# Kernel tuning notes

Measured on AMD Instinct MI355X. Metric: run time of the kernel, lower is better.

Reference implementation:

```python
import jax, jax.numpy as jnp
import numpy as np

# Constants matching init_kwargs
PC_MIN_X, PC_MIN_Y = -70.4, -40.0
VX, VY = 0.1, 0.1
RADII = (0.4, 0.8)
NSAMPLE = 16
EPS = 1e-5

B, K, N = 2, 2048, 16384
C_BEV, H_BEV, W_BEV = 256, 100, 176


def setup_inputs() -> dict:
    key = jax.random.key(0)
    ks = jax.random.split(key, 16)
    u = lambda k, s: jax.random.uniform(k, s, jnp.float32)
    kp = jnp.stack([
        u(ks[0], (B, K)) * 136.0 - 68.0,
        u(ks[1], (B, K)) * 76.0 - 38.0,
        u(ks[2], (B, K)) * 2.5 - 2.0,   # z in (-2.0, 0.5) -> kpt_mask all True
    ], axis=-1)
    pts = jnp.stack([
        u(ks[3], (B, N)) * 140.0 - 70.0,
        u(ks[4], (B, N)) * 80.0 - 40.0,
        u(ks[5], (B, N)) * 4.0 - 3.0,
    ], axis=-1)
    r = lambda k, s: jax.random.normal(k, s, jnp.float32)
    s01 = lambda k, s: r(k, s) * 0.1
    return {
        "keypoints": kp,
        "points_xyz": pts,
        "points_feat": r(ks[6], (B, N, 1)),
        "spatial_features": r(ks[7], (B, C_BEV, H_BEV, W_BEV)),
        "bev_stride": 8,
        "W0_s0": s01(ks[8], (16, 4)), "g0_s0": jnp.ones(16), "b0_s0": jnp.zeros(16),
        "W1_s0": s01(ks[9], (16, 16)), "g1_s0": jnp.ones(16), "b1_s0": jnp.zeros(16),
        "W0_s1": s01(ks[10], (16, 4)), "g0_s1": jnp.ones(16), "b0_s1": jnp.zeros(16),
        "W1_s1": s01(ks[11], (32, 16)), "g1_s1": jnp.ones(32), "b1_s1": jnp.zeros(32),
        "Wf": s01(ks[12], (128, 304)), "gf": jnp.ones(128), "bf": jnp.zeros(128),
    }


def _batchnorm(x, g, b, axes):
    m = x.mean(axes, keepdims=True)
    v = x.var(axes, keepdims=True)
    return (x - m) * jax.lax.rsqrt(v + EPS) * g + b


def _ball_group(dist2, xyz_b, feat_b, kp_b, radius, ns):
    """pcdet ball_query: first ns in-radius neighbors (index order), pad by first idx."""
    Kq, Np = dist2.shape
    within = dist2 < radius * radius                      # (K, N)
    order = jnp.cumsum(within, axis=1) - 1                # slot for each point
    valid = within & (order < ns)
    pos = jnp.where(valid, order, ns)                     # invalid -> overflow slot
    idx = jnp.zeros((Kq, ns + 1), jnp.int32)
    idx = idx.at[jnp.arange(Kq)[:, None], pos].set(
        jnp.broadcast_to(jnp.arange(Np, dtype=jnp.int32)[None, :], (Kq, Np)))
    idx = idx[:, :ns]
    cnt = within.sum(axis=1)
    slot_ok = jnp.arange(ns)[None, :] < cnt[:, None]
    idx = jnp.where(slot_ok, idx, idx[:, :1])             # replicate first found idx
    empty = cnt == 0
    grouped_xyz = xyz_b[idx] - kp_b[:, None, :]           # (K, ns, 3)
    grouped = jnp.concatenate([grouped_xyz, feat_b[idx]], axis=-1)  # (K, ns, 3+C)
    grouped = jnp.where(empty[:, None, None], 0.0, grouped)
    return grouped, empty


def _group_both_scales(xyz_b, feat_b, kp_b):
    # pairwise dist computed ONCE, shared across both radii
    dist2 = jnp.sum((kp_b[:, None, :] - xyz_b[None, :, :]) ** 2, axis=-1)  # (K, N)
    g0, e0 = _ball_group(dist2, xyz_b, feat_b, kp_b, RADII[0], NSAMPLE)
    g1, e1 = _ball_group(dist2, xyz_b, feat_b, kp_b, RADII[1], NSAMPLE)
    return g0, e0, g1, e1


def _shared_mlp_pool(grouped, empty, layers):
    x = grouped                                            # (B, K, ns, Cin)
    for (W, g, b) in layers:
        x = jnp.einsum('bknc,oc->bkno', x, W)
        x = _batchnorm(x, g, b, axes=(0, 1, 2))            # BN2d over stacked M*ns
        x = jax.nn.relu(x)
    pooled = x.max(axis=2)                                 # max over ns -> (B, K, Cout)
    return jnp.where(empty[:, :, None], 0.0, pooled)


def _bev_interp(bev, kp, stride):
    # bev: (B, C, H, W); kp: (B, K, 3)
    im = jnp.transpose(bev, (0, 2, 3, 1))                  # (B, H, W, C)
    x = (kp[..., 0] - PC_MIN_X) / VX / stride
    y = (kp[..., 1] - PC_MIN_Y) / VY / stride
    Hh, Ww = im.shape[1], im.shape[2]
    x0 = jnp.clip(jnp.floor(x).astype(jnp.int32), 0, Ww - 1)
    x1 = jnp.clip(jnp.floor(x).astype(jnp.int32) + 1, 0, Ww - 1)
    y0 = jnp.clip(jnp.floor(y).astype(jnp.int32), 0, Hh - 1)
    y1 = jnp.clip(jnp.floor(y).astype(jnp.int32) + 1, 0, Hh - 1)
    bidx = jnp.arange(im.shape[0])[:, None]
    Ia, Ib = im[bidx, y0, x0], im[bidx, y1, x0]
    Ic, Id = im[bidx, y0, x1], im[bidx, y1, x1]
    x0f, x1f = x0.astype(x.dtype), x1.astype(x.dtype)
    y0f, y1f = y0.astype(y.dtype), y1.astype(y.dtype)
    wa = ((x1f - x) * (y1f - y))[..., None]
    wb = ((x1f - x) * (y - y0f))[..., None]
    wc = ((x - x0f) * (y1f - y))[..., None]
    wd = ((x - x0f) * (y - y0f))[..., None]
    return Ia * wa + Ib * wb + Ic * wc + Id * wd           # (B, K, C)


def reference(keypoints, points_xyz, points_feat, spatial_features, bev_stride,
              W0_s0, g0_s0, b0_s0, W1_s0, g1_s0, b1_s0,
              W0_s1, g0_s1, b0_s1, W1_s1, g1_s1, b1_s1,
              Wf, gf, bf):
    Bb, Kk, _ = keypoints.shape
    # BEV bilinear interpolation
    bev_feat = _bev_interp(spatial_features, keypoints, bev_stride)  # (B, K, C_bev)
    # per-batch ball-query grouping (vmapped over batch)
    g0, e0, g1, e1 = jax.vmap(_group_both_scales)(points_xyz, points_feat, keypoints)
    p0 = _shared_mlp_pool(g0, e0, [(W0_s0, g0_s0, b0_s0), (W1_s0, g1_s0, b1_s0)])
    p1 = _shared_mlp_pool(g1, e1, [(W0_s1, g0_s1, b0_s1), (W1_s1, g1_s1, b1_s1)])
    pooled = jnp.concatenate([p0, p1], axis=-1)            # (B, K, 48)
    feats = jnp.concatenate([bev_feat, pooled], axis=-1).reshape(Bb * Kk, -1)  # (M, 304)
    # vsa_point_feature_fusion: Linear(no bias) + BN1d(train) + ReLU
    fused = feats @ Wf.T
    fused = jax.nn.relu(_batchnorm(fused, gf, bf, axes=(0,)))
    return fused                                           # (B*K, 128)
```

## Files before the change

kernel.cpp:

```cpp
#include <hip/hip_runtime.h>
#include <hip/hip_bf16.h>

#define NB    2
#define NK    2048
#define NPTS  16384
#define NBK   4096
#define MSAMP 65536.0f
#define MROW  4096.0f

#define NCELLX 176
#define NCELLY 101
#define NCELLS 17776
#define CAP    24

#define NREP   32
#define NCTR   64

#define AL(p) __hip_atomic_load((p), __ATOMIC_RELAXED, __HIP_MEMORY_SCOPE_AGENT)

#define ATOMIC_ADD_ACK(p, v) do { \
  float _r = atomicAdd((p), (v)); \
  asm volatile("" :: "v"(_r)); } while (0)

#define ACC14(M, w, X, Y, Z, F) do { \
  M[0] += (w)*(X); M[1] += (w)*(Y); M[2] += (w)*(Z); M[3] += (w)*(F); \
  M[4] += (w)*(X)*(X); M[5] += (w)*(X)*(Y); M[6] += (w)*(X)*(Z); M[7] += (w)*(X)*(F); \
  M[8] += (w)*(Y)*(Y); M[9] += (w)*(Y)*(Z); M[10] += (w)*(Y)*(F); \
  M[11] += (w)*(Z)*(Z); M[12] += (w)*(Z)*(F); M[13] += (w)*(F)*(F); } while (0)

__device__ __forceinline__ int cell_of(float x, float y) {
  int cx = (int)floorf((x + 70.4f) * 1.25f);
  int cy = (int)floorf((y + 40.0f) * 1.25f);
  cx = min(max(cx, 0), NCELLX - 1);
  cy = min(max(cy, 0), NCELLY - 1);
  return cy * NCELLX + cx;
}

__device__ __forceinline__ void grid_barrier(int* base, int per, int myc) {
  asm volatile("s_waitcnt vmcnt(0)" ::: "memory");
  __syncthreads();
  const int t = threadIdx.x;
  int* ctr = base;
  int* rel = base + NCTR;
  if (t == 0) {
    int old = __hip_atomic_fetch_add(&ctr[myc], 1, __ATOMIC_RELAXED,
                                     __HIP_MEMORY_SCOPE_AGENT);
    asm volatile("" :: "v"(old));
  }
  if (blockIdx.x == 0) {
    if (t < NCTR) {
      while (AL(&ctr[t]) < per) __builtin_amdgcn_s_sleep(8);
    }
    __syncthreads();
    if (t < NCTR)
      __hip_atomic_store(&rel[t], 1, __ATOMIC_RELAXED,
                         __HIP_MEMORY_SCOPE_AGENT);
  } else {
    if (t == 0) {
      while (AL(&rel[myc]) == 0) __builtin_amdgcn_s_sleep(8);
    }
  }
  __syncthreads();
}

__global__ __launch_bounds__(256) void bintrans_kernel(
    const float* __restrict__ pts, const float* __restrict__ pfeat,
    const float* __restrict__ bev,
    int* __restrict__ cellcnt, float4* __restrict__ bucketP,
    int* __restrict__ bucketI, float* __restrict__ bevT)
{
  __shared__ __align__(16) float ttile[64][65];
  const int t = threadIdx.x;
  const int wave = t >> 6;
  const int lane = t & 63;

  if (blockIdx.x < 128) {
    const int i  = blockIdx.x * 256 + t;
    const int b  = i >> 14;
    const int il = i & (NPTS - 1);
    const float* px = pts + (size_t)b * NPTS * 3;
    const float x = px[il*3+0], y = px[il*3+1], z = px[il*3+2];
    const float f = pfeat[(size_t)b * NPTS + il];
    const int c = b * NCELLS + cell_of(x, y);
    const int pos = atomicAdd(&cellcnt[c], 1);
    if (pos < CAP) {
      bucketP[(size_t)c * CAP + pos] = make_float4(x, y, z, f);
      bucketI[(size_t)c * CAP + pos] = il;
    }
    return;
  }

  const int tb  = blockIdx.x - 128;
  const int b   = tb / 1100;
  const int rem = tb % 1100;
  const int cg  = (rem / 275) * 64;
  const int sp0 = (rem % 275) * 64;
  #pragma unroll 4
  for (int i = 0; i < 16; i++) {
    const int c = cg + wave * 16 + i;
    ttile[wave * 16 + i][lane] = bev[((size_t)(b * 256 + c)) * 17600 + sp0 + lane];
  }
  __syncthreads();
  #pragma unroll 4
  for (int i = 0; i < 16; i++) {
    const int s = wave * 16 + i;
    bevT[((size_t)b * 17600 + sp0 + s) * 256 + cg + lane] = ttile[lane][s];
  }
}

__global__ __launch_bounds__(256, 2) void fused_kernel(
    const float* __restrict__ kp, const int* __restrict__ stridep,
    const float* __restrict__ bevT,
    const int* __restrict__ cellcnt, const float4* __restrict__ bucketP,
    const int* __restrict__ bucketI,
    const float* __restrict__ W0s0, const float* __restrict__ gm0s0, const float* __restrict__ bt0s0,
    const float* __restrict__ W0s1, const float* __restrict__ gm0s1, const float* __restrict__ bt0s1,
    const float* __restrict__ W1s0, const float* __restrict__ gm1s0, const float* __restrict__ bt1s0,
    const float* __restrict__ W1s1, const float* __restrict__ gm1s1, const float* __restrict__ bt1s1,
    const float* __restrict__ Wf, const float* __restrict__ gf, const float* __restrict__ bfp,
    float* __restrict__ S0r, float* __restrict__ S1r,
    float* __restrict__ S2sr, float* __restrict__ S2qr,
    int* __restrict__ ctrs, float* __restrict__ out)
{
  __shared__ float sW0a[64], sW0b[64], sW1a[256], sW1b[512], sP[160];
  __shared__ float skp[24];
  __shared__ float red[8][96];
  __shared__ float t2s[2][128], t2q[2][128];
  __shared__ float sA[128], sB[128];
  __shared__ __align__(16) float sF[8 * 304];
  __shared__ float4 sG0[8][16], sG1[8][16];
  __shared__ int scnt[2][8];
  const int t = threadIdx.x;
  const int bk0 = blockIdx.x * 8;
  const int rep = blockIdx.x & (NREP - 1);
  const int myc = blockIdx.x & (NCTR - 1);

  if (t < 24) skp[t] = kp[(size_t)bk0 * 3 + t];
  if (t < 64) { sW0a[t] = W0s0[t]; sW0b[t] = W0s1[t]; }
  sW1a[t]       = W1s0[t];
  sW1b[t]       = W1s1[t];
  sW1b[t + 256] = W1s1[t + 256];
  for (int i = t; i < 8 * 96; i += 256) ((float*)red)[i] = 0.f;
  __syncthreads();

  {
    const float st = (float)(*stridep);
    const int b = bk0 >> 11;
    const size_t pb = (size_t)b * 17600 * 256;
    #pragma unroll
    for (int r = 0; r < 8; r++) {
      const float x = (skp[r*3+0] - (-70.4f)) / 0.1f / st;
      const float y = (skp[r*3+1] - (-40.0f)) / 0.1f / st;
      const int xf = (int)floorf(x), yf = (int)floorf(y);
      const int x0 = min(max(xf, 0), 175), x1 = min(max(xf + 1, 0), 175);
      const int y0 = min(max(yf, 0), 99),  y1 = min(max(yf + 1, 0), 99);
      const float x0f = (float)x0, x1f = (float)x1, y0f = (float)y0, y1f = (float)y1;
      const float wa = (x1f - x) * (y1f - y);
      const float wb = (x1f - x) * (y - y0f);
      const float wc = (x - x0f) * (y1f - y);
      const float wd = (x - x0f) * (y - y0f);
      const float Ia = bevT[pb + (size_t)(y0 * 176 + x0) * 256 + t];
      const float Ib = bevT[pb + (size_t)(y1 * 176 + x0) * 256 + t];
      const float Ic = bevT[pb + (size_t)(y0 * 176 + x1) * 256 + t];
      const float Id = bevT[pb + (size_t)(y1 * 176 + x1) * 256 + t];
      sF[r * 304 + t] = Ia * wa + Ib * wb + Ic * wc + Id * wd;
    }
  }

  if (t < 8) {
    const int bk = bk0 + t;
    const int b  = bk >> 11;
    const float kx = skp[t*3+0], ky = skp[t*3+1], kz = skp[t*3+2];
    int cx = (int)floorf((kx + 70.4f) * 1.25f);
    int cy = (int)floorf((ky + 40.0f) * 1.25f);
    cx = min(max(cx, 1), NCELLX - 2);
    cy = min(max(cy, 1), NCELLY - 2);
    const int bcell = b * NCELLS;
    const int cb0 = bcell + (cy - 1) * NCELLX + cx - 1;

    int ncnt[9];
    #pragma unroll
    for (int r = 0; r < 3; r++)
      #pragma unroll
      for (int cc = 0; cc < 3; cc++)
        ncnt[r*3+cc] = min(cellcnt[cb0 + r * NCELLX + cc], CAP);

    int c0 = 0, c1 = 0;
    int mi0 = 0x7fffffff, mi1 = 0x7fffffff;
    float p0x = 0.f, p0y = 0.f, p0z = 0.f, p0f = 0.f;
    float p1x = 0.f, p1y = 0.f, p1z = 0.f, p1f = 0.f;
    float M0[14], M1[14];
    #pragma unroll
    for (int i = 0; i < 14; i++) { M0[i] = 0.f; M1[i] = 0.f; }

    #pragma unroll
    for (int r = 0; r < 3; r++) {
      #pragma unroll
      for (int cc = 0; cc < 3; cc++) {
        const int cell = cb0 + r * NCELLX + cc;
        const int n = ncnt[r*3+cc];
        const float4* bp = bucketP + (size_t)cell * CAP;
        const int*    bi = bucketI + (size_t)cell * CAP;
        for (int j = 0; j < n; ++j) {
          const float4 p = bp[j];
          const float dx = p.x - kx, dy = p.y - ky, dz = p.z - kz;
          const float d2 = dx*dx + dy*dy + dz*dz;
          if (d2 < 0.64f) {
            const int pi = bi[j];
            if (c1 < 16) {
              sG1[t][c1] = make_float4(dx, dy, dz, p.w);
              ACC14(M1, 1.0f, dx, dy, dz, p.w);
            }
            if (pi < mi1) { mi1 = pi; p1x = dx; p1y = dy; p1z = dz; p1f = p.w; }
            c1++;
            if (d2 < 0.16f) {
              if (c0 < 16) {
                sG0[t][c0] = make_float4(dx, dy, dz, p.w);
                ACC14(M0, 1.0f, dx, dy, dz, p.w);
              }
              if (pi < mi0) { mi0 = pi; p0x = dx; p0y = dy; p0z = dz; p0f = p.w; }
              c0++;
            }
          }
        }
      }
    }

    {
      const float4 v0 = make_float4(p0x, p0y, p0z, p0f);
      for (int s2 = c0; s2 < 16; ++s2) sG0[t][s2] = v0;
      const float w0 = (float)(16 - min(c0, 16));
      ACC14(M0, w0, p0x, p0y, p0z, p0f);
    }
    {
      const float4 v1 = make_float4(p1x, p1y, p1z, p1f);
      for (int s2 = c1; s2 < 16; ++s2) sG1[t][s2] = v1;
      const float w1 = (float)(16 - min(c1, 16));
      ACC14(M1, w1, p1x, p1y, p1z, p1f);
    }
    scnt[0][t] = c0;
    scnt[1][t] = c1;

    #pragma unroll
    for (int d = 1; d < 8; d <<= 1) {
      #pragma unroll
      for (int i = 0; i < 14; i++) {
        M0[i] += __shfl_xor(M0[i], d);
        M1[i] += __shfl_xor(M1[i], d);
      }
    }
    if (t == 0) {
      float* S0my = S0r + rep * 32;
      #pragma unroll
      for (int i = 0; i < 14; i++) {
        ATOMIC_ADD_ACK(&S0my[i],      M0[i]);
        ATOMIC_ADD_ACK(&S0my[14 + i], M1[i]);
      }
    }
  }

  grid_barrier(ctrs, 512 / NCTR, myc);

  if (t < 32) {
    const int s = t >> 4, c = t & 15;
    const float* W  = s ? sW0b : sW0a;
    const float* G  = s ? gm0s1 : gm0s0;
    const float* Bt = s ? bt0s1 : bt0s0;
    const float w0 = W[c*4+0], w1 = W[c*4+1];
    const float w2 = W[c*4+2], w3 = W[c*4+3];
    const float inv = 1.0f / MSAMP;
    float Sv[14];
    #pragma unroll
    for (int i = 0; i < 14; i++) {
      float a = 0.f;
      #pragma unroll
      for (int r = 0; r < NREP; r++) a += AL(S0r + r * 32 + s * 14 + i);
      Sv[i] = a;
    }
    const float mean = (w0*Sv[0] + w1*Sv[1] + w2*Sv[2] + w3*Sv[3]) * inv;
    float e2 = w0*w0*Sv[4] + 2.f*w0*w1*Sv[5] + 2.f*w0*w2*Sv[6] + 2.f*w0*w3*Sv[7]
             + w1*w1*Sv[8] + 2.f*w1*w2*Sv[9] + 2.f*w1*w3*Sv[10]
             + w2*w2*Sv[11] + 2.f*w2*w3*Sv[12] + w3*w3*Sv[13];
    e2 *= inv;
    const float var = e2 - mean * mean;
    const float A = G[c] / sqrtf(var + 1e-5f);
    sP[s*32 + c]      = A;
    sP[s*32 + 16 + c] = Bt[c] - mean * A;
  }
  __syncthreads();

  if (t < 128) {
    const int lkp = t >> 4, sl = t & 15;
    const int grp = t >> 4;
    const bool leader = (t & 15) == 0;
    float a1[16];
    {
      const float4 x = sG0[lkp][sl];
      #pragma unroll
      for (int c = 0; c < 16; c++) {
        const float h = sW0a[c*4+0]*x.x + sW0a[c*4+1]*x.y + sW0a[c*4+2]*x.z + sW0a[c*4+3]*x.w;
        a1[c] = fmaxf(fmaf(sP[c], h, sP[16+c]), 0.f);
      }
      #pragma unroll
      for (int o = 0; o < 16; o++) {
        float h2 = 0.f;
        #pragma unroll
        for (int c = 0; c < 16; c++) h2 = fmaf(sW1a[o*16+c], a1[c], h2);
        float s = h2, q = h2 * h2;
        #pragma unroll
        for (int d = 1; d < 16; d <<= 1) { s += __shfl_xor(s, d); q += __shfl_xor(q, d); }
        if (leader) { red[grp][o] += s; red[grp][16+o] += q; }
      }
    }
    {
      const float4 x = sG1[lkp][sl];
      #pragma unroll
      for (int c = 0; c < 16; c++) {
        const float h = sW0b[c*4+0]*x.x + sW0b[c*4+1]*x.y + sW0b[c*4+2]*x.z + sW0b[c*4+3]*x.w;
        a1[c] = fmaxf(fmaf(sP[32+c], h, sP[48+c]), 0.f);
      }
      #pragma unroll
      for (int o = 0; o < 32; o++) {
        float h2 = 0.f;
        #pragma unroll
        for (int c = 0; c < 16; c++) h2 = fmaf(sW1b[o*16+c], a1[c], h2);
        float s = h2, q = h2 * h2;
        #pragma unroll
        for (int d = 1; d < 16; d <<= 1) { s += __shfl_xor(s, d); q += __shfl_xor(q, d); }
        if (leader) { red[grp][32+o] += s; red[grp][64+o] += q; }
      }
    }
  }
  __syncthreads();
  if (t < 96) {
    float s = 0.f;
    #pragma unroll
    for (int g = 0; g < 8; g++) s += red[g][t];
    ATOMIC_ADD_ACK(&S1r[rep * 96 + t], s);
  }

  grid_barrier(ctrs + 2 * NCTR, 512 / NCTR, myc);

  if (t < 48) {
    float sum = 0.f, sq = 0.f, G, Bv; int oA, oB, os, oq;
    if (t < 16) { os = t; oq = 16 + t; G = gm1s0[t]; Bv = bt1s0[t]; oA = 64+t;  oB = 80+t; }
    else { const int c = t - 16; os = 32 + c; oq = 64 + c; G = gm1s1[c]; Bv = bt1s1[c]; oA = 96+c; oB = 128+c; }
    #pragma unroll
    for (int r = 0; r < NREP; r++) {
      sum += AL(S1r + r * 96 + os);
      sq  += AL(S1r + r * 96 + oq);
    }
    const float mean = sum / MSAMP;
    const float var  = sq / MSAMP - mean * mean;
    const float A = G / sqrtf(var + 1e-5f);
    sP[oA] = A;
    sP[oB] = Bv - mean * A;
  }
  __syncthreads();

  if (t < 128) {
    const int lkp = t >> 4, slot = t & 15;
    float a1[16], a2s0[16], a2s1[32];
    {
      const float4 x = sG0[lkp][slot];
      #pragma unroll
      for (int c = 0; c < 16; c++) {
        const float h = sW0a[c*4+0]*x.x + sW0a[c*4+1]*x.y + sW0a[c*4+2]*x.z + sW0a[c*4+3]*x.w;
        a1[c] = fmaxf(fmaf(sP[c], h, sP[16+c]), 0.f);
      }
      #pragma unroll
      for (int o = 0; o < 16; o++) {
        float h2 = 0.f;
        #pragma unroll
        for (int c = 0; c < 16; c++) h2 = fmaf(sW1a[o*16+c], a1[c], h2);
        a2s0[o] = fmaxf(fmaf(sP[64+o], h2, sP[80+o]), 0.f);
      }
    }
    {
      const float4 x = sG1[lkp][slot];
      #pragma unroll
      for (int c = 0; c < 16; c++) {
        const float h = sW0b[c*4+0]*x.x + sW0b[c*4+1]*x.y + sW0b[c*4+2]*x.z + sW0b[c*4+3]*x.w;
        a1[c] = fmaxf(fmaf(sP[32+c], h, sP[48+c]), 0.f);
      }
      #pragma unroll
      for (int o = 0; o < 32; o++) {
        float h2 = 0.f;
        #pragma unroll
        for (int c = 0; c < 16; c++) h2 = fmaf(sW1b[o*16+c], a1[c], h2);
        a2s1[o] = fmaxf(fmaf(sP[96+o], h2, sP[128+o]), 0.f);
      }
    }
    #pragma unroll
    for (int d = 1; d < 16; d <<= 1) {
      #pragma unroll
      for (int o = 0; o < 16; o++) a2s0[o] = fmaxf(a2s0[o], __shfl_xor(a2s0[o], d));
      #pragma unroll
      for (int o = 0; o < 32; o++) a2s1[o] = fmaxf(a2s1[o], __shfl_xor(a2s1[o], d));
    }
    if (slot == 0) {
      const int c0 = scnt[0][lkp], c1 = scnt[1][lkp];
      float* outp = sF + lkp * 304 + 256;
      #pragma unroll
      for (int o = 0; o < 16; o++) outp[o] = c0 ? a2s0[o] : 0.f;
      #pragma unroll
      for (int o = 0; o < 32; o++) outp[16 + o] = c1 ? a2s1[o] : 0.f;
    }
  }
  __syncthreads();

  const int c = t & 127;
  const int half = t >> 7;
  const int rbase = half * 4;
  float acc[4];
  {
    #pragma unroll
    for (int r = 0; r < 4; r++) acc[r] = 0.f;
    const float* wrow = Wf + (size_t)c * 304;
    for (int j4 = 0; j4 < 76; j4++) {
      const float4 w = *(const float4*)(wrow + j4 * 4);
      #pragma unroll
      for (int r = 0; r < 4; r++) {
        const float4 f = *(const float4*)(sF + (rbase + r) * 304 + j4 * 4);
        acc[r] = fmaf(w.x, f.x, acc[r]);
        acc[r] = fmaf(w.y, f.y, acc[r]);
        acc[r] = fmaf(w.z, f.z, acc[r]);
        acc[r] = fmaf(w.w, f.w, acc[r]);
      }
    }
    float s = 0.f, q = 0.f;
    #pragma unroll
    for (int r = 0; r < 4; r++) {
      s += acc[r];
      q = fmaf(acc[r], acc[r], q);
    }
    t2s[half][c] = s;
    t2q[half][c] = q;
  }
  __syncthreads();
  if (t < 128) {
    ATOMIC_ADD_ACK(&S2sr[rep * 128 + t], t2s[0][t] + t2s[1][t]);
    ATOMIC_ADD_ACK(&S2qr[rep * 128 + t], t2q[0][t] + t2q[1][t]);
  }

  grid_barrier(ctrs + 4 * NCTR, 512 / NCTR, myc);

  if (t < 128) {
    float s = 0.f, q = 0.f;
    #pragma unroll
    for (int r = 0; r < NREP; r++) {
      s += AL(S2sr + r * 128 + t);
      q += AL(S2qr + r * 128 + t);
    }
    const float mean = s / MROW;
    const float var  = q / MROW - mean * mean;
    const float A = gf[t] / sqrtf(var + 1e-5f);
    sA[t] = A;
    sB[t] = bfp[t] - mean * A;
  }
  __syncthreads();
  {
    const float A = sA[c], B = sB[c];
    #pragma unroll
    for (int r = 0; r < 4; r++) {
      out[(size_t)(bk0 + rbase + r) * 128 + c] = fmaxf(fmaf(acc[r], A, B), 0.f);
    }
  }
}

extern "C" void kernel_launch(void* const* d_in, const int* in_sizes, int n_in,
                              void* d_out, int out_size, void* d_ws, size_t ws_size,
                              hipStream_t stream)
{
  const float* kp    = (const float*)d_in[0];
  const float* pts   = (const float*)d_in[1];
  const float* pfeat = (const float*)d_in[2];
  const float* bev   = (const float*)d_in[3];
  const int*   strd  = (const int*)d_in[4];
  const float* W0s0  = (const float*)d_in[5];
  const float* g0s0  = (const float*)d_in[6];
  const float* b0s0  = (const float*)d_in[7];
  const float* W1s0  = (const float*)d_in[8];
  const float* g1s0  = (const float*)d_in[9];
  const float* b1s0  = (const float*)d_in[10];
  const float* W0s1  = (const float*)d_in[11];
  const float* g0s1  = (const float*)d_in[12];
  const float* b0s1  = (const float*)d_in[13];
  const float* W1s1  = (const float*)d_in[14];
  const float* g1s1  = (const float*)d_in[15];
  const float* b1s1  = (const float*)d_in[16];
  const float* Wf    = (const float*)d_in[17];
  const float* gf    = (const float*)d_in[18];
  const float* bfv   = (const float*)d_in[19];

  float* w = (float*)d_ws;
  int*   cellcnt = (int*)(w + 1048576);
  int*   ctrs    = cellcnt + 2 * NCELLS;
  float* S0r     = (float*)(ctrs + 6 * NCTR);
  float* S1r     = S0r + NREP * 32;
  float* S2sr    = S1r + NREP * 96;
  float* S2qr    = S2sr + NREP * 128;
  const size_t zero_elems = 2 * NCELLS + 6 * NCTR
                          + NREP * (32 + 96 + 128 + 128);

  float*  bevT    = w + 1245184;
  float4* bucketP = (float4*)(w + 10256384);
  int*    bucketI = (int*)(w + 10256384 + (size_t)2 * NCELLS * CAP * 4);

  hipMemsetAsync(cellcnt, 0, zero_elems * sizeof(int), stream);
  hipLaunchKernelGGL(bintrans_kernel, dim3(2328), dim3(256), 0, stream,
                     pts, pfeat, bev, cellcnt, bucketP, bucketI, bevT);
  hipLaunchKernelGGL(fused_kernel, dim3(512), dim3(256), 0, stream,
                     kp, strd, bevT, cellcnt, bucketP, bucketI,
                     W0s0, g0s0, b0s0, W0s1, g0s1, b0s1,
                     W1s0, g1s0, b1s0, W1s1, g1s1, b1s1,
                     Wf, gf, bfv, S0r, S1r, S2sr, S2qr, ctrs, (float*)d_out);
}
```

Measured before the change: 191.1 us.

## Parallelize candidate gathering, spread post-barrier reductions, and reuse layer-2 pre-activations

Neighbor candidate collection is split across 8 lanes per keypoint, which prefix-sum their cell counts and copy bucket points into a shared candidate list. A single lane per keypoint then scans that list from LDS instead of walking global buckets serially. After each grid barrier, the per-replica statistic reductions are spread over more threads with a two-stage LDS sum, which shortens the serial atomic-load chains. The second-layer pre-activations h2 are kept in registers across the barrier, so the final pass no longer recomputes the full MLP. The cost is extra LDS use, register pressure from 48 live floats, and candidate lists that are capped at 64 entries.

Result: faster. 183.8 us (-3.8%).

```diff
diff --git a/kernel.cpp b/kernel.cpp
--- a/kernel.cpp
+++ b/kernel.cpp
@@ -12,6 +12,7 @@
 #define NCELLY 101
 #define NCELLS 17776
 #define CAP    24
+#define CANDMAX 64
 
 #define NREP   32
 #define NCTR   64
@@ -127,8 +128,12 @@
   __shared__ float red[8][96];
   __shared__ float t2s[2][128], t2q[2][128];
   __shared__ float sA[128], sB[128];
+  __shared__ float s0p[8][28], sS0[28];
   __shared__ __align__(16) float sF[8 * 304];
   __shared__ float4 sG0[8][16], sG1[8][16];
+  __shared__ __align__(16) float4 sCand[8][CANDMAX];
+  __shared__ int sCandI[8][CANDMAX];
+  __shared__ int sTot[8];
   __shared__ int scnt[2][8];
   const int t = threadIdx.x;
   const int bk0 = blockIdx.x * 8;
@@ -167,23 +172,49 @@
     }
   }
 
-  if (t < 8) {
-    const int bk = bk0 + t;
-    const int b  = bk >> 11;
-    const float kx = skp[t*3+0], ky = skp[t*3+1], kz = skp[t*3+2];
+  if (t < 64) {
+    const int kpi = t >> 3, sub = t & 7;
+    const int b   = (bk0 + kpi) >> 11;
+    const float kx = skp[kpi*3+0], ky = skp[kpi*3+1];
     int cx = (int)floorf((kx + 70.4f) * 1.25f);
     int cy = (int)floorf((ky + 40.0f) * 1.25f);
     cx = min(max(cx, 1), NCELLX - 2);
     cy = min(max(cy, 1), NCELLY - 2);
-    const int bcell = b * NCELLS;
-    const int cb0 = bcell + (cy - 1) * NCELLX + cx - 1;
-
-    int ncnt[9];
-    #pragma unroll
-    for (int r = 0; r < 3; r++)
-      #pragma unroll
-      for (int cc = 0; cc < 3; cc++)
-        ncnt[r*3+cc] = min(cellcnt[cb0 + r * NCELLX + cc], CAP);
+    const int cb0 = b * NCELLS + (cy - 1) * NCELLX + cx - 1;
+    const int cellS = cb0 + (sub / 3) * NCELLX + (sub % 3);
+    const int cell8 = cb0 + 2 * NCELLX + 2;
+    const int nS = min(cellcnt[cellS], CAP);
+    const int n8 = (sub == 0) ? min(cellcnt[cell8], CAP) : 0;
+    int pre = nS;
+    #pragma unroll
+    for (int d = 1; d < 8; d <<= 1) {
+      const int v = __shfl_up(pre, d, 8);
+      if (sub >= d) pre += v;
+    }
+    const int offS  = pre - nS;
+    const int tot07 = __shfl(pre, 7, 8);
+    const float4* bp = bucketP + (size_t)cellS * CAP;
+    const int*    bi = bucketI + (size_t)cellS * CAP;
+    for (int j = 0; j < nS; ++j) {
+      const int o = offS + j;
+      if (o < CANDMAX) { sCand[kpi][o] = bp[j]; sCandI[kpi][o] = bi[j]; }
+    }
+    if (sub == 0) {
+      const float4* bp8 = bucketP + (size_t)cell8 * CAP;
+      const int*    bi8 = bucketI + (size_t)cell8 * CAP;
+      for (int j = 0; j < n8; ++j) {
+        const int o = tot07 + j;
+        if (o < CANDMAX) { sCand[kpi][o] = bp8[j]; sCandI[kpi][o] = bi8[j]; }
+      }
+      sTot[kpi] = min(tot07 + n8, CANDMAX);
+    }
+  }
+  __syncthreads();
+
+  if (t < 64 && (t & 7) == 0) {
+    const int kpi = t >> 3;
+    const float kx = skp[kpi*3+0], ky = skp[kpi*3+1], kz = skp[kpi*3+2];
+    const int T = sTot[kpi];
 
     int c0 = 0, c1 = 0;
     int mi0 = 0x7fffffff, mi1 = 0x7fffffff;
@@ -193,56 +224,46 @@
     #pragma unroll
     for (int i = 0; i < 14; i++) { M0[i] = 0.f; M1[i] = 0.f; }
 
-    #pragma unroll
-    for (int r = 0; r < 3; r++) {
-      #pragma unroll
-      for (int cc = 0; cc < 3; cc++) {
-        const int cell = cb0 + r * NCELLX + cc;
-        const int n = ncnt[r*3+cc];
-        const float4* bp = bucketP + (size_t)cell * CAP;
-        const int*    bi = bucketI + (size_t)cell * CAP;
-        for (int j = 0; j < n; ++j) {
-          const float4 p = bp[j];
-          const float dx = p.x - kx, dy = p.y - ky, dz = p.z - kz;
-          const float d2 = dx*dx + dy*dy + dz*dz;
-          if (d2 < 0.64f) {
-            const int pi = bi[j];
-            if (c1 < 16) {
-              sG1[t][c1] = make_float4(dx, dy, dz, p.w);
-              ACC14(M1, 1.0f, dx, dy, dz, p.w);
-            }
-            if (pi < mi1) { mi1 = pi; p1x = dx; p1y = dy; p1z = dz; p1f = p.w; }
-            c1++;
-            if (d2 < 0.16f) {
-              if (c0 < 16) {
-                sG0[t][c0] = make_float4(dx, dy, dz, p.w);
-                ACC14(M0, 1.0f, dx, dy, dz, p.w);
-              }
-              if (pi < mi0) { mi0 = pi; p0x = dx; p0y = dy; p0z = dz; p0f = p.w; }
-              c0++;
-            }
+    for (int j = 0; j < T; ++j) {
+      const float4 p = sCand[kpi][j];
+      const float dx = p.x - kx, dy = p.y - ky, dz = p.z - kz;
+      const float d2 = dx*dx + dy*dy + dz*dz;
+      if (d2 < 0.64f) {
+        const int pi = sCandI[kpi][j];
+        if (c1 < 16) {
+          sG1[kpi][c1] = make_float4(dx, dy, dz, p.w);
+          ACC14(M1, 1.0f, dx, dy, dz, p.w);
+        }
+        if (pi < mi1) { mi1 = pi; p1x = dx; p1y = dy; p1z = dz; p1f = p.w; }
+        c1++;
+        if (d2 < 0.16f) {
+          if (c0 < 16) {
+            sG0[kpi][c0] = make_float4(dx, dy, dz, p.w);
+            ACC14(M0, 1.0f, dx, dy, dz, p.w);
           }
+          if (pi < mi0) { mi0 = pi; p0x = dx; p0y = dy; p0z = dz; p0f = p.w; }
+          c0++;
         }
       }
     }
 
     {
       const float4 v0 = make_float4(p0x, p0y, p0z, p0f);
-      for (int s2 = c0; s2 < 16; ++s2) sG0[t][s2] = v0;
+      for (int s2 = c0; s2 < 16; ++s2) sG0[kpi][s2] = v0;
       const float w0 = (float)(16 - min(c0, 16));
       ACC14(M0, w0, p0x, p0y, p0z, p0f);
     }
     {
       const float4 v1 = make_float4(p1x, p1y, p1z, p1f);
-      for (int s2 = c1; s2 < 16; ++s2) sG1[t][s2] = v1;
+      for (int s2 = c1; s2 < 16; ++s2) sG1[kpi][s2] = v1;
       const float w1 = (float)(16 - min(c1, 16));
       ACC14(M1, w1, p1x, p1y, p1z, p1f);
     }
-    scnt[0][t] = c0;
-    scnt[1][t] = c1;
-
-    #pragma unroll
-    for (int d = 1; d < 8; d <<= 1) {
+    scnt[0][kpi] = c0;
+    scnt[1][kpi] = c1;
+
+    #pragma unroll
+    for (int d = 8; d < 64; d <<= 1) {
       #pragma unroll
       for (int i = 0; i < 14; i++) {
         M0[i] += __shfl_xor(M0[i], d);
@@ -261,26 +282,34 @@
 
   grid_barrier(ctrs, 512 / NCTR, myc);
 
+  if (t < 224) {
+    const int m = t % 28, g = t / 28;
+    float a = 0.f;
+    #pragma unroll
+    for (int r2 = 0; r2 < 4; r2++) a += AL(S0r + (g * 4 + r2) * 32 + m);
+    s0p[g][m] = a;
+  }
+  __syncthreads();
+  if (t < 28) {
+    float a = 0.f;
+    #pragma unroll
+    for (int g = 0; g < 8; g++) a += s0p[g][t];
+    sS0[t] = a;
+  }
+  __syncthreads();
   if (t < 32) {
     const int s = t >> 4, c = t & 15;
     const float* W  = s ? sW0b : sW0a;
     const float* G  = s ? gm0s1 : gm0s0;
     const float* Bt = s ? bt0s1 : bt0s0;
+    const float* Sx = sS0 + s * 14;
     const float w0 = W[c*4+0], w1 = W[c*4+1];
     const float w2 = W[c*4+2], w3 = W[c*4+3];
     const float inv = 1.0f / MSAMP;
-    float Sv[14];
-    #pragma unroll
-    for (int i = 0; i < 14; i++) {
-      float a = 0.f;
-      #pragma unroll
-      for (int r = 0; r < NREP; r++) a += AL(S0r + r * 32 + s * 14 + i);
-      Sv[i] = a;
-    }
-    const float mean = (w0*Sv[0] + w1*Sv[1] + w2*Sv[2] + w3*Sv[3]) * inv;
-    float e2 = w0*w0*Sv[4] + 2.f*w0*w1*Sv[5] + 2.f*w0*w2*Sv[6] + 2.f*w0*w3*Sv[7]
-             + w1*w1*Sv[8] + 2.f*w1*w2*Sv[9] + 2.f*w1*w3*Sv[10]
-             + w2*w2*Sv[11] + 2.f*w2*w3*Sv[12] + w3*w3*Sv[13];
+    const float mean = (w0*Sx[0] + w1*Sx[1] + w2*Sx[2] + w3*Sx[3]) * inv;
+    float e2 = w0*w0*Sx[4] + 2.f*w0*w1*Sx[5] + 2.f*w0*w2*Sx[6] + 2.f*w0*w3*Sx[7]
+             + w1*w1*Sx[8] + 2.f*w1*w2*Sx[9] + 2.f*w1*w3*Sx[10]
+             + w2*w2*Sx[11] + 2.f*w2*w3*Sx[12] + w3*w3*Sx[13];
     e2 *= inv;
     const float var = e2 - mean * mean;
     const float A = G[c] / sqrtf(var + 1e-5f);
@@ -289,6 +318,7 @@
   }
   __syncthreads();
 
+  float h2a[16], h2b[32];
   if (t < 128) {
     const int lkp = t >> 4, sl = t & 15;
     const int grp = t >> 4;
@@ -306,6 +336,7 @@
         float h2 = 0.f;
         #pragma unroll
         for (int c = 0; c < 16; c++) h2 = fmaf(sW1a[o*16+c], a1[c], h2);
+        h2a[o] = h2;
         float s = h2, q = h2 * h2;
         #pragma unroll
         for (int d = 1; d < 16; d <<= 1) { s += __shfl_xor(s, d); q += __shfl_xor(q, d); }
@@ -324,6 +355,7 @@
         float h2 = 0.f;
         #pragma unroll
         for (int c = 0; c < 16; c++) h2 = fmaf(sW1b[o*16+c], a1[c], h2);
+        h2b[o] = h2;
         float s = h2, q = h2 * h2;
         #pragma unroll
         for (int d = 1; d < 16; d <<= 1) { s += __shfl_xor(s, d); q += __shfl_xor(q, d); }
@@ -341,15 +373,20 @@
 
   grid_barrier(ctrs + 2 * NCTR, 512 / NCTR, myc);
 
+  if (t < 192) {
+    const int v = t % 96, h = t / 96;
+    float a = 0.f;
+    #pragma unroll
+    for (int r2 = 0; r2 < 16; r2++) a += AL(S1r + (h * 16 + r2) * 96 + v);
+    red[h][v] = a;
+  }
+  __syncthreads();
   if (t < 48) {
-    float sum = 0.f, sq = 0.f, G, Bv; int oA, oB, os, oq;
+    float sum, sq, G, Bv; int oA, oB, os, oq;
     if (t < 16) { os = t; oq = 16 + t; G = gm1s0[t]; Bv = bt1s0[t]; oA = 64+t;  oB = 80+t; }
     else { const int c = t - 16; os = 32 + c; oq = 64 + c; G = gm1s1[c]; Bv = bt1s1[c]; oA = 96+c; oB = 128+c; }
-    #pragma unroll
-    for (int r = 0; r < NREP; r++) {
-      sum += AL(S1r + r * 96 + os);
-      sq  += AL(S1r + r * 96 + oq);
-    }
+    sum = red[0][os] + red[1][os];
+    sq  = red[0][oq] + red[1][oq];
     const float mean = sum / MSAMP;
     const float var  = sq / MSAMP - mean * mean;
     const float A = G / sqrtf(var + 1e-5f);
@@ -360,37 +397,11 @@
 
   if (t < 128) {
     const int lkp = t >> 4, slot = t & 15;
-    float a1[16], a2s0[16], a2s1[32];
-    {
-      const float4 x = sG0[lkp][slot];
-      #pragma unroll
-      for (int c = 0; c < 16; c++) {
-        const float h = sW0a[c*4+0]*x.x + sW0a[c*4+1]*x.y + sW0a[c*4+2]*x.z + sW0a[c*4+3]*x.w;
-        a1[c] = fmaxf(fmaf(sP[c], h, sP[16+c]), 0.f);
-      }
-      #pragma unroll
-      for (int o = 0; o < 16; o++) {
-        float h2 = 0.f;
-        #pragma unroll
-        for (int c = 0; c < 16; c++) h2 = fmaf(sW1a[o*16+c], a1[c], h2);
-        a2s0[o] = fmaxf(fmaf(sP[64+o], h2, sP[80+o]), 0.f);
-      }
-    }
-    {
-      const float4 x = sG1[lkp][slot];
-      #pragma unroll
-      for (int c = 0; c < 16; c++) {
-        const float h = sW0b[c*4+0]*x.x + sW0b[c*4+1]*x.y + sW0b[c*4+2]*x.z + sW0b[c*4+3]*x.w;
-        a1[c] = fmaxf(fmaf(sP[32+c], h, sP[48+c]), 0.f);
-      }
-      #pragma unroll
-      for (int o = 0; o < 32; o++) {
-        float h2 = 0.f;
-        #pragma unroll
-        for (int c = 0; c < 16; c++) h2 = fmaf(sW1b[o*16+c], a1[c], h2);
-        a2s1[o] = fmaxf(fmaf(sP[96+o], h2, sP[128+o]), 0.f);
-      }
-    }
+    float a2s0[16], a2s1[32];
+    #pragma unroll
+    for (int o = 0; o < 16; o++) a2s0[o] = fmaxf(fmaf(sP[64+o], h2a[o], sP[80+o]), 0.f);
+    #pragma unroll
+    for (int o = 0; o < 32; o++) a2s1[o] = fmaxf(fmaf(sP[96+o], h2b[o], sP[128+o]), 0.f);
     #pragma unroll
     for (int d = 1; d < 16; d <<= 1) {
       #pragma unroll
@@ -445,15 +456,18 @@
 
   grid_barrier(ctrs + 4 * NCTR, 512 / NCTR, myc);
 
+  {
+    const int v = t & 127;
+    const float* Sx = (t < 128) ? S2sr : S2qr;
+    float a = 0.f;
+    #pragma unroll
+    for (int r = 0; r < NREP; r++) a += AL(Sx + r * 128 + v);
+    if (t < 128) t2s[0][v] = a; else t2q[0][v] = a;
+  }
+  __syncthreads();
   if (t < 128) {
-    float s = 0.f, q = 0.f;
-    #pragma unroll
-    for (int r = 0; r < NREP; r++) {
-      s += AL(S2sr + r * 128 + t);
-      q += AL(S2qr + r * 128 + t);
-    }
-    const float mean = s / MROW;
-    const float var  = q / MROW - mean * mean;
+    const float mean = t2s[0][t] / MROW;
+    const float var  = t2q[0][t] / MROW - mean * mean;
     const float A = gf[t] / sqrtf(var + 1e-5f);
     sA[t] = A;
     sB[t] = bfp[t] - mean * A;
```
